# Optimization experiments

Measured on AMD Instinct MI355X. Metric: run time of the kernel, lower is better.

## Reference

```python
import jax, jax.numpy as jnp
import numpy as np
import math

D_MODEL = 2048
D_STATE = 16
EXPAND = 2
D_INNER = D_MODEL * EXPAND          # 4096
DT_RANK = math.ceil(D_MODEL / 16)   # 128
BATCH, SEQ_LEN = 2, 512


def setup_inputs() -> dict:
    key = jax.random.key(0)
    ks = jax.random.split(key, 6)
    x = jax.random.normal(ks[0], (BATCH, SEQ_LEN, D_INNER), dtype=jnp.float32)
    # A_log such that A = -exp(A_log) is a stable negative-real decay
    A_log = jnp.log(jax.random.uniform(ks[1], (D_INNER, D_STATE), minval=0.5, maxval=16.0, dtype=jnp.float32))
    D = jnp.ones((D_INNER,), dtype=jnp.float32)
    x_proj_w = 0.02 * jax.random.normal(ks[2], (DT_RANK + 2 * D_STATE, D_INNER), dtype=jnp.float32)
    dt_init_std = DT_RANK ** -0.5
    dt_proj_w = jax.random.uniform(ks[3], (D_INNER, DT_RANK), minval=-dt_init_std, maxval=dt_init_std, dtype=jnp.float32)
    # inverse-softplus init of dt bias, dt ~ loguniform[1e-3, 0.1]
    dt = jnp.exp(jax.random.uniform(ks[4], (D_INNER,), dtype=jnp.float32) * (math.log(0.1) - math.log(0.001)) + math.log(0.001))
    dt = jnp.clip(dt, 1e-4, None)
    dt_proj_b = dt + jnp.log(-jnp.expm1(-dt))
    return {"x": x, "A_log": A_log, "D": D, "x_proj_w": x_proj_w,
            "dt_proj_w": dt_proj_w, "dt_proj_b": dt_proj_b}


def reference(x, A_log, D, x_proj_w, dt_proj_w, dt_proj_b):
    # x: (b, l, d)
    A = -jnp.exp(A_log)                                  # (d, n)
    xp = jnp.einsum('bld,rd->blr', x, x_proj_w)          # (b, l, dt_rank + 2n)
    dt_in = xp[..., :DT_RANK]
    B = xp[..., DT_RANK:DT_RANK + D_STATE]               # (b, l, n)
    C = xp[..., DT_RANK + D_STATE:]                      # (b, l, n)
    dt = jax.nn.softplus(jnp.einsum('blr,dr->bld', dt_in, dt_proj_w) + dt_proj_b)  # (b, l, d)
    dA = jnp.exp(dt[..., None] * A)                      # (b, l, d, n)
    dBx = dt[..., None] * B[:, :, None, :] * x[..., None]  # (b, l, d, n)

    def step(h, inp):
        dA_t, dBx_t, C_t = inp                           # (b,d,n), (b,d,n), (b,n)
        h = dA_t * h + dBx_t
        y = jnp.einsum('bdn,bn->bd', h, C_t)
        return h, y

    h0 = jnp.zeros((x.shape[0], D_INNER, D_STATE), dtype=x.dtype)
    _, ys = jax.lax.scan(step, h0,
                         (jnp.moveaxis(dA, 1, 0), jnp.moveaxis(dBx, 1, 0), jnp.moveaxis(C, 1, 0)))
    y = jnp.moveaxis(ys, 0, 1) + D * x                   # (b, l, d)
    return y
```

## Files before the change

### kernel.cpp

```cpp
#include <hip/hip_runtime.h>
#include <math.h>

#define BATCH   2
#define SEQLEN  512
#define DI      4096
#define DS      16
#define RDT     128
#define RTOT    160
#define BL      1024

#define KSPLIT  32
#define KSL     (DI / KSPLIT)

typedef __bf16 bf16;
typedef bf16  bf16x8 __attribute__((ext_vector_type(8)));
typedef bf16  bf16x4 __attribute__((ext_vector_type(4)));
typedef float f32x4  __attribute__((ext_vector_type(4)));

__global__ __launch_bounds__(256) void cast_both(const float* __restrict__ W,
                                                 const float* __restrict__ dtw,
                                                 bf16* __restrict__ Wb,
                                                 bf16* __restrict__ dtwb) {
  const int i = blockIdx.x * 256 + threadIdx.x;
  const float4* src;
  bf16* dst;
  int j;
  if (i < RTOT * DI / 4) { src = (const float4*)W;   dst = Wb;   j = i; }
  else                   { src = (const float4*)dtw; dst = dtwb; j = i - RTOT * DI / 4; }
  float4 v = src[j];
  bf16x4 o;
  o[0] = (bf16)v.x; o[1] = (bf16)v.y; o[2] = (bf16)v.z; o[3] = (bf16)v.w;
  *(bf16x4*)(dst + 4 * (size_t)j) = o;
}

__global__ __launch_bounds__(256) void gemm_xp_mfma(const float* __restrict__ x,
                                                    const bf16* __restrict__ Wb,
                                                    float* __restrict__ part) {
  const int tid = threadIdx.x;
  const int w = tid >> 6;
  const int lane = tid & 63;
  const int m = lane & 15;
  const int q = lane >> 4;
  const int row0 = blockIdx.x * 64 + 16 * w;
  const int k0 = blockIdx.y * KSL;

  f32x4 acc[10] = {};

  const float* ap = x + (size_t)(row0 + m) * DI + k0 + 8 * q;
  const bf16*  bp = Wb + (size_t)m * DI + k0 + 8 * q;

#pragma unroll
  for (int kk = 0; kk < KSL; kk += 32) {
    float4 a0 = *(const float4*)(ap + kk);
    float4 a1 = *(const float4*)(ap + kk + 4);
    bf16x8 af;
    af[0] = (bf16)a0.x; af[1] = (bf16)a0.y; af[2] = (bf16)a0.z; af[3] = (bf16)a0.w;
    af[4] = (bf16)a1.x; af[5] = (bf16)a1.y; af[6] = (bf16)a1.z; af[7] = (bf16)a1.w;
#pragma unroll
    for (int nt = 0; nt < 10; ++nt) {
      bf16x8 bfv = *(const bf16x8*)(bp + (size_t)nt * 16 * DI + kk);
      acc[nt] = __builtin_amdgcn_mfma_f32_16x16x32_bf16(af, bfv, acc[nt], 0, 0, 0);
    }
  }

  float* p = part + (size_t)blockIdx.y * (BL * RTOT);
#pragma unroll
  for (int nt = 0; nt < 10; ++nt)
#pragma unroll
    for (int r = 0; r < 4; ++r)
      p[(size_t)(row0 + 4 * q + r) * RTOT + nt * 16 + m] = acc[nt][r];
}

__global__ __launch_bounds__(256) void reduce_xp(const float* __restrict__ part,
                                                 float* __restrict__ BCf,
                                                 bf16* __restrict__ dtinb) {
  const int o = (blockIdx.x * 256 + threadIdx.x) * 4;
  float4 s = make_float4(0.f, 0.f, 0.f, 0.f);
#pragma unroll
  for (int k = 0; k < KSPLIT; ++k) {
    float4 v = *(const float4*)&part[(size_t)k * (BL * RTOT) + o];
    s.x += v.x; s.y += v.y; s.z += v.z; s.w += v.w;
  }
  const int row = o / RTOT;
  const int col = o - row * RTOT;
  if (col < RDT) {
    bf16x4 ob;
    ob[0] = (bf16)s.x; ob[1] = (bf16)s.y; ob[2] = (bf16)s.z; ob[3] = (bf16)s.w;
    *(bf16x4*)(dtinb + (size_t)row * RDT + col) = ob;
  } else {
    *(float4*)&BCf[(size_t)row * 32 + (col - RDT)] = s;
  }
}

__device__ __forceinline__ float row16_reduce_add(float p) {
  p += __int_as_float(__builtin_amdgcn_update_dpp(
      0, __float_as_int(p), 0x111, 0xf, 0xf, true));
  p += __int_as_float(__builtin_amdgcn_update_dpp(
      0, __float_as_int(p), 0x112, 0xf, 0xf, true));
  p += __int_as_float(__builtin_amdgcn_update_dpp(
      0, __float_as_int(p), 0x114, 0xf, 0xf, true));
  p += __int_as_float(__builtin_amdgcn_update_dpp(
      0, __float_as_int(p), 0x118, 0xf, 0xf, true));
  return p;
}

#define TC  64
#define TCP 68
#define NCH (SEQLEN / TC)

__global__ __launch_bounds__(256) void scan_fused(const float* __restrict__ x,
                                                  const float* __restrict__ A_log,
                                                  const float* __restrict__ Dvec,
                                                  const float* __restrict__ BCf,
                                                  const bf16* __restrict__ dtin,
                                                  const bf16* __restrict__ dtwb,
                                                  const float* __restrict__ dtb,
                                                  float* __restrict__ out) {
  __shared__ __align__(16) float dtS[16][TCP];
  __shared__ __align__(16) float xS[16][TCP];
  __shared__ __align__(16) float BS[16][TCP];
  __shared__ __align__(16) float CS[16][TCP];
  __shared__ __align__(16) float yS[TC][16];

  const int bid = blockIdx.x;
  const int b = bid >> 8;
  const int d0 = (bid & 255) * 16;
  const int tid = threadIdx.x;
  const int n = tid & 15;
  const int dc = tid >> 4;
  const int d = d0 + dc;
  const int w = tid >> 6;
  const int m = tid & 15;
  const int q = (tid >> 4) & 3;

  const float A = -expf(A_log[d * DS + n]);
  const float Dd = Dvec[d];
  const float bias = dtb[d0 + m];

  bf16x8 bfragW[4];
#pragma unroll
  for (int k = 0; k < 4; ++k)
    bfragW[k] = *(const bf16x8*)(dtwb + (size_t)(d0 + m) * RDT + 32 * k + 8 * q);

  const int lt = tid >> 2;
  const int lf = (tid & 3) * 4;
  const int rowbase = b * SEQLEN;

  bf16x8 afrag[4];
  float4 rx, rB, rC;
  {
    const int arow = rowbase + 16 * w + m;
#pragma unroll
    for (int k = 0; k < 4; ++k)
      afrag[k] = *(const bf16x8*)(dtin + (size_t)arow * RDT + 32 * k + 8 * q);
    const int row = rowbase + lt;
    rx = *(const float4*)&x[(size_t)row * DI + d0 + lf];
    rB = *(const float4*)&BCf[row * 32 + lf];
    rC = *(const float4*)&BCf[row * 32 + 16 + lf];
  }

  float h = 0.f;

  for (int c = 0; c < NCH; ++c) {
    if (c > 0) __syncthreads();

    {
      f32x4 acc = {};
#pragma unroll
      for (int k = 0; k < 4; ++k)
        acc = __builtin_amdgcn_mfma_f32_16x16x32_bf16(afrag[k], bfragW[k], acc, 0, 0, 0);
#pragma unroll
      for (int r = 0; r < 4; ++r) {
        const float z = acc[r] + bias;
        dtS[m][16 * w + 4 * q + r] = (z > 20.f) ? z : __logf(1.f + __expf(z));
      }
    }
    {
      const float rxa[4] = {rx.x, rx.y, rx.z, rx.w};
      const float rBa[4] = {rB.x, rB.y, rB.z, rB.w};
      const float rCa[4] = {rC.x, rC.y, rC.z, rC.w};
#pragma unroll
      for (int j = 0; j < 4; ++j) {
        xS[lf + j][lt] = rxa[j];
        BS[lf + j][lt] = rBa[j];
        CS[lf + j][lt] = rCa[j];
      }
    }
    if (c > 0) {
      const int prow = rowbase + (c - 1) * TC + lt;
      float4 yv = *(const float4*)&yS[lt][lf];
      *(float4*)&out[(size_t)prow * DI + d0 + lf] = yv;
    }

    __syncthreads();

    if (c < NCH - 1) {
      const int arow = rowbase + (c + 1) * TC + 16 * w + m;
#pragma unroll
      for (int k = 0; k < 4; ++k)
        afrag[k] = *(const bf16x8*)(dtin + (size_t)arow * RDT + 32 * k + 8 * q);
      const int row = rowbase + (c + 1) * TC + lt;
      rx = *(const float4*)&x[(size_t)row * DI + d0 + lf];
      rB = *(const float4*)&BCf[row * 32 + lf];
      rC = *(const float4*)&BCf[row * 32 + 16 + lf];
    }

    for (int g = 0; g < 8; ++g) {
      const int t0 = 8 * g;
      const float4 dv0 = *(const float4*)&dtS[dc][t0];
      const float4 dv1 = *(const float4*)&dtS[dc][t0 + 4];
      const float4 xv0 = *(const float4*)&xS[dc][t0];
      const float4 xv1 = *(const float4*)&xS[dc][t0 + 4];
      const float4 Bv0 = *(const float4*)&BS[n][t0];
      const float4 Bv1 = *(const float4*)&BS[n][t0 + 4];
      const float4 Cv0 = *(const float4*)&CS[n][t0];
      const float4 Cv1 = *(const float4*)&CS[n][t0 + 4];
      const float dt[8] = {dv0.x, dv0.y, dv0.z, dv0.w, dv1.x, dv1.y, dv1.z, dv1.w};
      const float xv[8] = {xv0.x, xv0.y, xv0.z, xv0.w, xv1.x, xv1.y, xv1.z, xv1.w};
      const float Bv[8] = {Bv0.x, Bv0.y, Bv0.z, Bv0.w, Bv1.x, Bv1.y, Bv1.z, Bv1.w};
      const float Cv[8] = {Cv0.x, Cv0.y, Cv0.z, Cv0.w, Cv1.x, Cv1.y, Cv1.z, Cv1.w};

      float e[8], u[8], p[8];
#pragma unroll
      for (int j = 0; j < 8; ++j) {
        e[j] = __expf(dt[j] * A);
        u[j] = dt[j] * xv[j] * Bv[j];
      }
#pragma unroll
      for (int j = 0; j < 8; ++j) {
        h = fmaf(e[j], h, u[j]);
        p[j] = h * Cv[j];
      }
#pragma unroll
      for (int j = 0; j < 8; ++j)
        p[j] = row16_reduce_add(p[j]);
      if (n == 15) {
#pragma unroll
        for (int j = 0; j < 8; ++j)
          yS[t0 + j][dc] = fmaf(Dd, xv[j], p[j]);
      }
    }
  }

  __syncthreads();
  {
    const int prow = rowbase + (NCH - 1) * TC + lt;
    float4 yv = *(const float4*)&yS[lt][lf];
    *(float4*)&out[(size_t)prow * DI + d0 + lf] = yv;
  }
}

extern "C" void kernel_launch(void* const* d_in, const int* in_sizes, int n_in,
                              void* d_out, int out_size, void* d_ws, size_t ws_size,
                              hipStream_t stream) {
  const float* x     = (const float*)d_in[0];
  const float* A_log = (const float*)d_in[1];
  const float* Dv    = (const float*)d_in[2];
  const float* W     = (const float*)d_in[3];
  const float* dtw   = (const float*)d_in[4];
  const float* dtb   = (const float*)d_in[5];
  float* out = (float*)d_out;

  char* ws = (char*)d_ws;
  float* part  = (float*)ws;
  bf16*  Wb    = (bf16*)(ws + 20971520);
  bf16*  dtwb  = (bf16*)(ws + 22282240);
  float* BCf   = (float*)(ws + 23330816);
  bf16*  dtinb = (bf16*)(ws + 23461888);

  cast_both<<<dim3(1152), 256, 0, stream>>>(W, dtw, Wb, dtwb);
  gemm_xp_mfma<<<dim3(16, KSPLIT), 256, 0, stream>>>(x, Wb, part);
  reduce_xp<<<dim3(160), 256, 0, stream>>>(part, BCf, dtinb);
  scan_fused<<<dim3(512), 256, 0, stream>>>(x, A_log, Dv, BCf, dtinb, dtwb, dtb, out);
}
```

Baseline: 136.0 us.

## Fuse GEMM, reduce and scan into one cooperative kernel with grid syncs

Replaces the four separate launches (weight cast, split-K GEMM, reduce, scan) with a single cooperative kernel of 256 blocks of 512 threads. Each block runs two 256-thread virtual blocks, and grid.sync separates the GEMM, reduce and scan phases. The separate bf16 cast kernel is removed, so fp32 weights are converted to bf16 inline inside the GEMM and the scan. The aim is to cut launch overhead and inter-kernel gaps. In exchange it adds grid-barrier cost, twice the fp32 weight reads, and occupancy limits from the 512-thread blocks, and it falls back to three kernels if the cooperative launch fails.

```diff
diff --git a/kernel.cpp b/kernel.cpp
--- a/kernel.cpp
+++ b/kernel.cpp
@@ -1,5 +1,8 @@
 #include <hip/hip_runtime.h>
+#include <hip/hip_cooperative_groups.h>
 #include <math.h>
+
+namespace cg = cooperative_groups;
 
 #define BATCH   2
 #define SEQLEN  512
@@ -12,85 +15,14 @@
 #define KSPLIT  32
 #define KSL     (DI / KSPLIT)
 
+#define TC  64
+#define TCP 68
+#define NCH (SEQLEN / TC)
+
 typedef __bf16 bf16;
 typedef bf16  bf16x8 __attribute__((ext_vector_type(8)));
 typedef bf16  bf16x4 __attribute__((ext_vector_type(4)));
 typedef float f32x4  __attribute__((ext_vector_type(4)));
-
-__global__ __launch_bounds__(256) void cast_both(const float* __restrict__ W,
-                                                 const float* __restrict__ dtw,
-                                                 bf16* __restrict__ Wb,
-                                                 bf16* __restrict__ dtwb) {
-  const int i = blockIdx.x * 256 + threadIdx.x;
-  const float4* src;
-  bf16* dst;
-  int j;
-  if (i < RTOT * DI / 4) { src = (const float4*)W;   dst = Wb;   j = i; }
-  else                   { src = (const float4*)dtw; dst = dtwb; j = i - RTOT * DI / 4; }
-  float4 v = src[j];
-  bf16x4 o;
-  o[0] = (bf16)v.x; o[1] = (bf16)v.y; o[2] = (bf16)v.z; o[3] = (bf16)v.w;
-  *(bf16x4*)(dst + 4 * (size_t)j) = o;
-}
-
-__global__ __launch_bounds__(256) void gemm_xp_mfma(const float* __restrict__ x,
-                                                    const bf16* __restrict__ Wb,
-                                                    float* __restrict__ part) {
-  const int tid = threadIdx.x;
-  const int w = tid >> 6;
-  const int lane = tid & 63;
-  const int m = lane & 15;
-  const int q = lane >> 4;
-  const int row0 = blockIdx.x * 64 + 16 * w;
-  const int k0 = blockIdx.y * KSL;
-
-  f32x4 acc[10] = {};
-
-  const float* ap = x + (size_t)(row0 + m) * DI + k0 + 8 * q;
-  const bf16*  bp = Wb + (size_t)m * DI + k0 + 8 * q;
-
-#pragma unroll
-  for (int kk = 0; kk < KSL; kk += 32) {
-    float4 a0 = *(const float4*)(ap + kk);
-    float4 a1 = *(const float4*)(ap + kk + 4);
-    bf16x8 af;
-    af[0] = (bf16)a0.x; af[1] = (bf16)a0.y; af[2] = (bf16)a0.z; af[3] = (bf16)a0.w;
-    af[4] = (bf16)a1.x; af[5] = (bf16)a1.y; af[6] = (bf16)a1.z; af[7] = (bf16)a1.w;
-#pragma unroll
-    for (int nt = 0; nt < 10; ++nt) {
-      bf16x8 bfv = *(const bf16x8*)(bp + (size_t)nt * 16 * DI + kk);
-      acc[nt] = __builtin_amdgcn_mfma_f32_16x16x32_bf16(af, bfv, acc[nt], 0, 0, 0);
-    }
-  }
-
-  float* p = part + (size_t)blockIdx.y * (BL * RTOT);
-#pragma unroll
-  for (int nt = 0; nt < 10; ++nt)
-#pragma unroll
-    for (int r = 0; r < 4; ++r)
-      p[(size_t)(row0 + 4 * q + r) * RTOT + nt * 16 + m] = acc[nt][r];
-}
-
-__global__ __launch_bounds__(256) void reduce_xp(const float* __restrict__ part,
-                                                 float* __restrict__ BCf,
-                                                 bf16* __restrict__ dtinb) {
-  const int o = (blockIdx.x * 256 + threadIdx.x) * 4;
-  float4 s = make_float4(0.f, 0.f, 0.f, 0.f);
-#pragma unroll
-  for (int k = 0; k < KSPLIT; ++k) {
-    float4 v = *(const float4*)&part[(size_t)k * (BL * RTOT) + o];
-    s.x += v.x; s.y += v.y; s.z += v.z; s.w += v.w;
-  }
-  const int row = o / RTOT;
-  const int col = o - row * RTOT;
-  if (col < RDT) {
-    bf16x4 ob;
-    ob[0] = (bf16)s.x; ob[1] = (bf16)s.y; ob[2] = (bf16)s.z; ob[3] = (bf16)s.w;
-    *(bf16x4*)(dtinb + (size_t)row * RDT + col) = ob;
-  } else {
-    *(float4*)&BCf[(size_t)row * 32 + (col - RDT)] = s;
-  }
-}
 
 __device__ __forceinline__ float row16_reduce_add(float p) {
   p += __int_as_float(__builtin_amdgcn_update_dpp(
@@ -104,34 +36,100 @@
   return p;
 }
 
-#define TC  64
-#define TCP 68
-#define NCH (SEQLEN / TC)
-
-__global__ __launch_bounds__(256) void scan_fused(const float* __restrict__ x,
-                                                  const float* __restrict__ A_log,
-                                                  const float* __restrict__ Dvec,
-                                                  const float* __restrict__ BCf,
-                                                  const bf16* __restrict__ dtin,
-                                                  const bf16* __restrict__ dtwb,
-                                                  const float* __restrict__ dtb,
-                                                  float* __restrict__ out) {
-  __shared__ __align__(16) float dtS[16][TCP];
-  __shared__ __align__(16) float xS[16][TCP];
-  __shared__ __align__(16) float BS[16][TCP];
-  __shared__ __align__(16) float CS[16][TCP];
-  __shared__ __align__(16) float yS[TC][16];
-
-  const int bid = blockIdx.x;
-  const int b = bid >> 8;
-  const int d0 = (bid & 255) * 16;
-  const int tid = threadIdx.x;
-  const int n = tid & 15;
-  const int dc = tid >> 4;
+__device__ __forceinline__ bf16x8 cvt_bf16x8(float4 a0, float4 a1) {
+  bf16x8 r;
+  r[0] = (bf16)a0.x; r[1] = (bf16)a0.y; r[2] = (bf16)a0.z; r[3] = (bf16)a0.w;
+  r[4] = (bf16)a1.x; r[5] = (bf16)a1.y; r[6] = (bf16)a1.z; r[7] = (bf16)a1.w;
+  return r;
+}
+
+struct __align__(16) ScanLds {
+  float dtS[16][TCP];
+  float xS[16][TCP];
+  float BS[16][TCP];
+  float CS[16][TCP];
+  float yS[TC][16];
+};
+
+__device__ __forceinline__ void phaseB_gemm(const float* __restrict__ x,
+                                            const float* __restrict__ W,
+                                            float* __restrict__ part,
+                                            int vb, int t) {
+  const int w4 = t >> 6;
+  const int lane = t & 63;
+  const int m = lane & 15;
+  const int q = lane >> 4;
+  const int mb = vb >> 5;
+  const int ks = vb & 31;
+  const int row0 = mb * 64 + 16 * w4;
+  const int k0 = ks * KSL;
+
+  f32x4 acc[10] = {};
+  const float* ap = x + (size_t)(row0 + m) * DI + k0 + 8 * q;
+  const float* bp = W + (size_t)m * DI + k0 + 8 * q;
+
+#pragma unroll
+  for (int kk = 0; kk < KSL; kk += 32) {
+    float4 a0 = *(const float4*)(ap + kk);
+    float4 a1 = *(const float4*)(ap + kk + 4);
+    bf16x8 af = cvt_bf16x8(a0, a1);
+#pragma unroll
+    for (int nt = 0; nt < 10; ++nt) {
+      float4 b0 = *(const float4*)(bp + (size_t)nt * 16 * DI + kk);
+      float4 b1 = *(const float4*)(bp + (size_t)nt * 16 * DI + kk + 4);
+      bf16x8 bfv = cvt_bf16x8(b0, b1);
+      acc[nt] = __builtin_amdgcn_mfma_f32_16x16x32_bf16(af, bfv, acc[nt], 0, 0, 0);
+    }
+  }
+  float* pp = part + (size_t)ks * (BL * RTOT);
+#pragma unroll
+  for (int nt = 0; nt < 10; ++nt)
+#pragma unroll
+    for (int r = 0; r < 4; ++r)
+      pp[(size_t)(row0 + 4 * q + r) * RTOT + nt * 16 + m] = acc[nt][r];
+}
+
+__device__ __forceinline__ void phaseC_reduce(const float* __restrict__ part,
+                                              float* __restrict__ BCf,
+                                              bf16* __restrict__ dtinb,
+                                              int gtid) {
+  if (gtid >= BL * RTOT / 4) return;
+  const int o = gtid * 4;
+  float4 s = make_float4(0.f, 0.f, 0.f, 0.f);
+#pragma unroll
+  for (int k = 0; k < KSPLIT; ++k) {
+    float4 v = *(const float4*)&part[(size_t)k * (BL * RTOT) + o];
+    s.x += v.x; s.y += v.y; s.z += v.z; s.w += v.w;
+  }
+  const int row = o / RTOT;
+  const int col = o - row * RTOT;
+  if (col < RDT) {
+    bf16x4 ob;
+    ob[0] = (bf16)s.x; ob[1] = (bf16)s.y; ob[2] = (bf16)s.z; ob[3] = (bf16)s.w;
+    *(bf16x4*)(dtinb + (size_t)row * RDT + col) = ob;
+  } else {
+    *(float4*)&BCf[(size_t)row * 32 + (col - RDT)] = s;
+  }
+}
+
+__device__ __forceinline__ void phaseD_scan(ScanLds& L,
+                                            const float* __restrict__ x,
+                                            const float* __restrict__ A_log,
+                                            const float* __restrict__ Dvec,
+                                            const float* __restrict__ BCf,
+                                            const bf16* __restrict__ dtin,
+                                            const float* __restrict__ dtw,
+                                            const float* __restrict__ dtb,
+                                            float* __restrict__ out,
+                                            int group, int t) {
+  const int b = group >> 8;
+  const int d0 = (group & 255) * 16;
+  const int n = t & 15;
+  const int dc = t >> 4;
   const int d = d0 + dc;
-  const int w = tid >> 6;
-  const int m = tid & 15;
-  const int q = (tid >> 4) & 3;
+  const int w = t >> 6;
+  const int m = t & 15;
+  const int q = (t >> 4) & 3;
 
   const float A = -expf(A_log[d * DS + n]);
   const float Dd = Dvec[d];
@@ -139,11 +137,13 @@
 
   bf16x8 bfragW[4];
 #pragma unroll
-  for (int k = 0; k < 4; ++k)
-    bfragW[k] = *(const bf16x8*)(dtwb + (size_t)(d0 + m) * RDT + 32 * k + 8 * q);
-
-  const int lt = tid >> 2;
-  const int lf = (tid & 3) * 4;
+  for (int k = 0; k < 4; ++k) {
+    const float* wp = dtw + (size_t)(d0 + m) * RDT + 32 * k + 8 * q;
+    bfragW[k] = cvt_bf16x8(*(const float4*)wp, *(const float4*)(wp + 4));
+  }
+
+  const int lt = t >> 2;
+  const int lf = (t & 3) * 4;
   const int rowbase = b * SEQLEN;
 
   bf16x8 afrag[4];
@@ -172,7 +172,7 @@
 #pragma unroll
       for (int r = 0; r < 4; ++r) {
         const float z = acc[r] + bias;
-        dtS[m][16 * w + 4 * q + r] = (z > 20.f) ? z : __logf(1.f + __expf(z));
+        L.dtS[m][16 * w + 4 * q + r] = (z > 20.f) ? z : __logf(1.f + __expf(z));
       }
     }
     {
@@ -181,14 +181,14 @@
       const float rCa[4] = {rC.x, rC.y, rC.z, rC.w};
 #pragma unroll
       for (int j = 0; j < 4; ++j) {
-        xS[lf + j][lt] = rxa[j];
-        BS[lf + j][lt] = rBa[j];
-        CS[lf + j][lt] = rCa[j];
+        L.xS[lf + j][lt] = rxa[j];
+        L.BS[lf + j][lt] = rBa[j];
+        L.CS[lf + j][lt] = rCa[j];
       }
     }
     if (c > 0) {
       const int prow = rowbase + (c - 1) * TC + lt;
-      float4 yv = *(const float4*)&yS[lt][lf];
+      float4 yv = *(const float4*)&L.yS[lt][lf];
       *(float4*)&out[(size_t)prow * DI + d0 + lf] = yv;
     }
 
@@ -207,14 +207,14 @@
 
     for (int g = 0; g < 8; ++g) {
       const int t0 = 8 * g;
-      const float4 dv0 = *(const float4*)&dtS[dc][t0];
-      const float4 dv1 = *(const float4*)&dtS[dc][t0 + 4];
-      const float4 xv0 = *(const float4*)&xS[dc][t0];
-      const float4 xv1 = *(const float4*)&xS[dc][t0 + 4];
-      const float4 Bv0 = *(const float4*)&BS[n][t0];
-      const float4 Bv1 = *(const float4*)&BS[n][t0 + 4];
-      const float4 Cv0 = *(const float4*)&CS[n][t0];
-      const float4 Cv1 = *(const float4*)&CS[n][t0 + 4];
+      const float4 dv0 = *(const float4*)&L.dtS[dc][t0];
+      const float4 dv1 = *(const float4*)&L.dtS[dc][t0 + 4];
+      const float4 xv0 = *(const float4*)&L.xS[dc][t0];
+      const float4 xv1 = *(const float4*)&L.xS[dc][t0 + 4];
+      const float4 Bv0 = *(const float4*)&L.BS[n][t0];
+      const float4 Bv1 = *(const float4*)&L.BS[n][t0 + 4];
+      const float4 Cv0 = *(const float4*)&L.CS[n][t0];
+      const float4 Cv1 = *(const float4*)&L.CS[n][t0 + 4];
       const float dt[8] = {dv0.x, dv0.y, dv0.z, dv0.w, dv1.x, dv1.y, dv1.z, dv1.w};
       const float xv[8] = {xv0.x, xv0.y, xv0.z, xv0.w, xv1.x, xv1.y, xv1.z, xv1.w};
       const float Bv[8] = {Bv0.x, Bv0.y, Bv0.z, Bv0.w, Bv1.x, Bv1.y, Bv1.z, Bv1.w};
@@ -237,7 +237,7 @@
       if (n == 15) {
 #pragma unroll
         for (int j = 0; j < 8; ++j)
-          yS[t0 + j][dc] = fmaf(Dd, xv[j], p[j]);
+          L.yS[t0 + j][dc] = fmaf(Dd, xv[j], p[j]);
       }
     }
   }
@@ -245,9 +245,60 @@
   __syncthreads();
   {
     const int prow = rowbase + (NCH - 1) * TC + lt;
-    float4 yv = *(const float4*)&yS[lt][lf];
+    float4 yv = *(const float4*)&L.yS[lt][lf];
     *(float4*)&out[(size_t)prow * DI + d0 + lf] = yv;
   }
+}
+
+__global__ __launch_bounds__(512, 2) void fused_all(
+    const float* __restrict__ x,     const float* __restrict__ A_log,
+    const float* __restrict__ Dvec,  const float* __restrict__ W,
+    const float* __restrict__ dtw,   const float* __restrict__ dtb,
+    float* __restrict__ part,        float* __restrict__ BCf,
+    bf16* __restrict__ dtinb,        float* __restrict__ out) {
+  __shared__ ScanLds L[2];
+  const int tid = threadIdx.x;
+  const int bid = blockIdx.x;
+  const int half = tid >> 8;
+  const int t = tid & 255;
+
+  cg::grid_group grid = cg::this_grid();
+
+  phaseB_gemm(x, W, part, bid * 2 + half, t);
+
+  __threadfence();
+  grid.sync();
+
+  phaseC_reduce(part, BCf, dtinb, bid * 512 + tid);
+
+  __threadfence();
+  grid.sync();
+
+  phaseD_scan(L[half], x, A_log, Dvec, BCf, dtinb, dtw, dtb, out,
+              bid * 2 + half, t);
+}
+
+__global__ __launch_bounds__(512, 2) void fb_gemm(const float* __restrict__ x,
+                                                  const float* __restrict__ W,
+                                                  float* __restrict__ part) {
+  phaseB_gemm(x, W, part, blockIdx.x * 2 + (threadIdx.x >> 8), threadIdx.x & 255);
+}
+
+__global__ __launch_bounds__(512) void fb_reduce(const float* __restrict__ part,
+                                                 float* __restrict__ BCf,
+                                                 bf16* __restrict__ dtinb) {
+  phaseC_reduce(part, BCf, dtinb, blockIdx.x * 512 + threadIdx.x);
+}
+
+__global__ __launch_bounds__(512, 2) void fb_scan(
+    const float* __restrict__ x, const float* __restrict__ A_log,
+    const float* __restrict__ Dvec, const float* __restrict__ BCf,
+    const bf16* __restrict__ dtin, const float* __restrict__ dtw,
+    const float* __restrict__ dtb, float* __restrict__ out) {
+  __shared__ ScanLds L[2];
+  const int half = threadIdx.x >> 8;
+  phaseD_scan(L[half], x, A_log, Dvec, BCf, dtin, dtw, dtb, out,
+              blockIdx.x * 2 + half, threadIdx.x & 255);
 }
 
 extern "C" void kernel_launch(void* const* d_in, const int* in_sizes, int n_in,
@@ -263,13 +314,17 @@
 
   char* ws = (char*)d_ws;
   float* part  = (float*)ws;
-  bf16*  Wb    = (bf16*)(ws + 20971520);
-  bf16*  dtwb  = (bf16*)(ws + 22282240);
-  float* BCf   = (float*)(ws + 23330816);
-  bf16*  dtinb = (bf16*)(ws + 23461888);
-
-  cast_both<<<dim3(1152), 256, 0, stream>>>(W, dtw, Wb, dtwb);
-  gemm_xp_mfma<<<dim3(16, KSPLIT), 256, 0, stream>>>(x, Wb, part);
-  reduce_xp<<<dim3(160), 256, 0, stream>>>(part, BCf, dtinb);
-  scan_fused<<<dim3(512), 256, 0, stream>>>(x, A_log, Dv, BCf, dtinb, dtwb, dtb, out);
-}
+  float* BCf   = (float*)(ws + 20971520);
+  bf16*  dtinb = (bf16*)(ws + 21102592);
+
+  void* args[] = {(void*)&x, (void*)&A_log, (void*)&Dv, (void*)&W, (void*)&dtw,
+                  (void*)&dtb, (void*)&part, (void*)&BCf, (void*)&dtinb, (void*)&out};
+  hipError_t err = hipLaunchCooperativeKernel((void*)fused_all, dim3(256),
+                                              dim3(512), args, 0, stream);
+  if (err != hipSuccess) {
+    (void)hipGetLastError();
+    fb_gemm<<<dim3(256), 512, 0, stream>>>(x, W, part);
+    fb_reduce<<<dim3(80), 512, 0, stream>>>(part, BCf, dtinb);
+    fb_scan<<<dim3(256), 512, 0, stream>>>(x, A_log, Dv, BCf, dtinb, dtw, dtb, out);
+  }
+}
```

New measurement: 343.6 us. 2.53x slower.

## Fuse weight cast, split-K GEMM and reduction into one in-block reduced GEMM

Applied to the files above, without the earlier changes.

Drops the separate weight-cast and partial-sum reduction kernels. The x-projection GEMM now runs as 64 blocks of 512 threads, where each of the 8 waves covers a 512-wide K slice and the partial sums are combined through shared memory in a tree before writing BCf and dt_in directly. The fp32 weights are converted to bf16 on the fly in both the GEMM and the scan kernel. This removes two launches and about 20MB of partial-sum traffic. In exchange, the GEMM grid shrinks from 512 blocks to 64, so many CUs may sit idle, and W is re-read in fp32 by every block.

```diff
diff --git a/kernel.cpp b/kernel.cpp
--- a/kernel.cpp
+++ b/kernel.cpp
@@ -9,111 +9,125 @@
 #define RTOT    160
 #define BL      1024
 
-#define KSPLIT  32
-#define KSL     (DI / KSPLIT)
+#define TC  64
+#define TCP 68
+#define NCH (SEQLEN / TC)
 
 typedef __bf16 bf16;
 typedef bf16  bf16x8 __attribute__((ext_vector_type(8)));
 typedef bf16  bf16x4 __attribute__((ext_vector_type(4)));
 typedef float f32x4  __attribute__((ext_vector_type(4)));
 
-__global__ __launch_bounds__(256) void cast_both(const float* __restrict__ W,
-                                                 const float* __restrict__ dtw,
-                                                 bf16* __restrict__ Wb,
-                                                 bf16* __restrict__ dtwb) {
-  const int i = blockIdx.x * 256 + threadIdx.x;
-  const float4* src;
-  bf16* dst;
-  int j;
-  if (i < RTOT * DI / 4) { src = (const float4*)W;   dst = Wb;   j = i; }
-  else                   { src = (const float4*)dtw; dst = dtwb; j = i - RTOT * DI / 4; }
-  float4 v = src[j];
-  bf16x4 o;
-  o[0] = (bf16)v.x; o[1] = (bf16)v.y; o[2] = (bf16)v.z; o[3] = (bf16)v.w;
-  *(bf16x4*)(dst + 4 * (size_t)j) = o;
-}
-
-__global__ __launch_bounds__(256) void gemm_xp_mfma(const float* __restrict__ x,
-                                                    const bf16* __restrict__ Wb,
-                                                    float* __restrict__ part) {
+__device__ __forceinline__ float row16_reduce_add(float p) {
+  p += __int_as_float(__builtin_amdgcn_update_dpp(
+      0, __float_as_int(p), 0x111, 0xf, 0xf, true));
+  p += __int_as_float(__builtin_amdgcn_update_dpp(
+      0, __float_as_int(p), 0x112, 0xf, 0xf, true));
+  p += __int_as_float(__builtin_amdgcn_update_dpp(
+      0, __float_as_int(p), 0x114, 0xf, 0xf, true));
+  p += __int_as_float(__builtin_amdgcn_update_dpp(
+      0, __float_as_int(p), 0x118, 0xf, 0xf, true));
+  return p;
+}
+
+__device__ __forceinline__ bf16x8 cvt_bf16x8(float4 a0, float4 a1) {
+  bf16x8 r;
+  r[0] = (bf16)a0.x; r[1] = (bf16)a0.y; r[2] = (bf16)a0.z; r[3] = (bf16)a0.w;
+  r[4] = (bf16)a1.x; r[5] = (bf16)a1.y; r[6] = (bf16)a1.z; r[7] = (bf16)a1.w;
+  return r;
+}
+
+__global__ __launch_bounds__(512) void gemm_fused(const float* __restrict__ x,
+                                                  const float* __restrict__ W,
+                                                  float* __restrict__ BCf,
+                                                  bf16* __restrict__ dtinb) {
+  __shared__ __align__(16) float img[4][16][164];
   const int tid = threadIdx.x;
   const int w = tid >> 6;
   const int lane = tid & 63;
   const int m = lane & 15;
   const int q = lane >> 4;
-  const int row0 = blockIdx.x * 64 + 16 * w;
-  const int k0 = blockIdx.y * KSL;
+  const int row0 = blockIdx.x * 16;
+  const int k0 = w * 512;
 
   f32x4 acc[10] = {};
-
   const float* ap = x + (size_t)(row0 + m) * DI + k0 + 8 * q;
-  const bf16*  bp = Wb + (size_t)m * DI + k0 + 8 * q;
-
-#pragma unroll
-  for (int kk = 0; kk < KSL; kk += 32) {
+  const float* bp = W + (size_t)m * DI + k0 + 8 * q;
+
+#pragma unroll 4
+  for (int kk = 0; kk < 512; kk += 32) {
     float4 a0 = *(const float4*)(ap + kk);
     float4 a1 = *(const float4*)(ap + kk + 4);
-    bf16x8 af;
-    af[0] = (bf16)a0.x; af[1] = (bf16)a0.y; af[2] = (bf16)a0.z; af[3] = (bf16)a0.w;
-    af[4] = (bf16)a1.x; af[5] = (bf16)a1.y; af[6] = (bf16)a1.z; af[7] = (bf16)a1.w;
+    bf16x8 af = cvt_bf16x8(a0, a1);
 #pragma unroll
     for (int nt = 0; nt < 10; ++nt) {
-      bf16x8 bfv = *(const bf16x8*)(bp + (size_t)nt * 16 * DI + kk);
+      float4 b0 = *(const float4*)(bp + (size_t)nt * 16 * DI + kk);
+      float4 b1 = *(const float4*)(bp + (size_t)nt * 16 * DI + kk + 4);
+      bf16x8 bfv = cvt_bf16x8(b0, b1);
       acc[nt] = __builtin_amdgcn_mfma_f32_16x16x32_bf16(af, bfv, acc[nt], 0, 0, 0);
     }
   }
 
-  float* p = part + (size_t)blockIdx.y * (BL * RTOT);
-#pragma unroll
-  for (int nt = 0; nt < 10; ++nt)
-#pragma unroll
-    for (int r = 0; r < 4; ++r)
-      p[(size_t)(row0 + 4 * q + r) * RTOT + nt * 16 + m] = acc[nt][r];
-}
-
-__global__ __launch_bounds__(256) void reduce_xp(const float* __restrict__ part,
-                                                 float* __restrict__ BCf,
-                                                 bf16* __restrict__ dtinb) {
-  const int o = (blockIdx.x * 256 + threadIdx.x) * 4;
-  float4 s = make_float4(0.f, 0.f, 0.f, 0.f);
-#pragma unroll
-  for (int k = 0; k < KSPLIT; ++k) {
-    float4 v = *(const float4*)&part[(size_t)k * (BL * RTOT) + o];
-    s.x += v.x; s.y += v.y; s.z += v.z; s.w += v.w;
-  }
-  const int row = o / RTOT;
-  const int col = o - row * RTOT;
-  if (col < RDT) {
-    bf16x4 ob;
-    ob[0] = (bf16)s.x; ob[1] = (bf16)s.y; ob[2] = (bf16)s.z; ob[3] = (bf16)s.w;
-    *(bf16x4*)(dtinb + (size_t)row * RDT + col) = ob;
-  } else {
-    *(float4*)&BCf[(size_t)row * 32 + (col - RDT)] = s;
-  }
-}
-
-__device__ __forceinline__ float row16_reduce_add(float p) {
-  p += __int_as_float(__builtin_amdgcn_update_dpp(
-      0, __float_as_int(p), 0x111, 0xf, 0xf, true));
-  p += __int_as_float(__builtin_amdgcn_update_dpp(
-      0, __float_as_int(p), 0x112, 0xf, 0xf, true));
-  p += __int_as_float(__builtin_amdgcn_update_dpp(
-      0, __float_as_int(p), 0x114, 0xf, 0xf, true));
-  p += __int_as_float(__builtin_amdgcn_update_dpp(
-      0, __float_as_int(p), 0x118, 0xf, 0xf, true));
-  return p;
-}
-
-#define TC  64
-#define TCP 68
-#define NCH (SEQLEN / TC)
+  if (w >= 4) {
+#pragma unroll
+    for (int nt = 0; nt < 10; ++nt)
+#pragma unroll
+      for (int r = 0; r < 4; ++r)
+        img[w - 4][4 * q + r][nt * 16 + m] = acc[nt][r];
+  }
+  __syncthreads();
+  if (w < 4) {
+#pragma unroll
+    for (int nt = 0; nt < 10; ++nt)
+#pragma unroll
+      for (int r = 0; r < 4; ++r)
+        acc[nt][r] += img[w][4 * q + r][nt * 16 + m];
+  }
+  __syncthreads();
+  if (w == 2 || w == 3) {
+#pragma unroll
+    for (int nt = 0; nt < 10; ++nt)
+#pragma unroll
+      for (int r = 0; r < 4; ++r)
+        img[w - 2][4 * q + r][nt * 16 + m] = acc[nt][r];
+  }
+  __syncthreads();
+  if (w < 2) {
+#pragma unroll
+    for (int nt = 0; nt < 10; ++nt)
+#pragma unroll
+      for (int r = 0; r < 4; ++r)
+        acc[nt][r] += img[w][4 * q + r][nt * 16 + m];
+  }
+  __syncthreads();
+  if (w == 1) {
+#pragma unroll
+    for (int nt = 0; nt < 10; ++nt)
+#pragma unroll
+      for (int r = 0; r < 4; ++r)
+        img[0][4 * q + r][nt * 16 + m] = acc[nt][r];
+  }
+  __syncthreads();
+  if (w == 0) {
+#pragma unroll
+    for (int nt = 0; nt < 10; ++nt)
+#pragma unroll
+      for (int r = 0; r < 4; ++r) {
+        const float v = acc[nt][r] + img[0][4 * q + r][nt * 16 + m];
+        const int row = row0 + 4 * q + r;
+        const int col = nt * 16 + m;
+        if (col < RDT) dtinb[(size_t)row * RDT + col] = (bf16)v;
+        else           BCf[(size_t)row * 32 + (col - RDT)] = v;
+      }
+  }
+}
 
 __global__ __launch_bounds__(256) void scan_fused(const float* __restrict__ x,
                                                   const float* __restrict__ A_log,
                                                   const float* __restrict__ Dvec,
                                                   const float* __restrict__ BCf,
                                                   const bf16* __restrict__ dtin,
-                                                  const bf16* __restrict__ dtwb,
+                                                  const float* __restrict__ dtw,
                                                   const float* __restrict__ dtb,
                                                   float* __restrict__ out) {
   __shared__ __align__(16) float dtS[16][TCP];
@@ -139,8 +153,10 @@
 
   bf16x8 bfragW[4];
 #pragma unroll
-  for (int k = 0; k < 4; ++k)
-    bfragW[k] = *(const bf16x8*)(dtwb + (size_t)(d0 + m) * RDT + 32 * k + 8 * q);
+  for (int k = 0; k < 4; ++k) {
+    const float* wp = dtw + (size_t)(d0 + m) * RDT + 32 * k + 8 * q;
+    bfragW[k] = cvt_bf16x8(*(const float4*)wp, *(const float4*)(wp + 4));
+  }
 
   const int lt = tid >> 2;
   const int lf = (tid & 3) * 4;
@@ -262,14 +278,9 @@
   float* out = (float*)d_out;
 
   char* ws = (char*)d_ws;
-  float* part  = (float*)ws;
-  bf16*  Wb    = (bf16*)(ws + 20971520);
-  bf16*  dtwb  = (bf16*)(ws + 22282240);
-  float* BCf   = (float*)(ws + 23330816);
-  bf16*  dtinb = (bf16*)(ws + 23461888);
-
-  cast_both<<<dim3(1152), 256, 0, stream>>>(W, dtw, Wb, dtwb);
-  gemm_xp_mfma<<<dim3(16, KSPLIT), 256, 0, stream>>>(x, Wb, part);
-  reduce_xp<<<dim3(160), 256, 0, stream>>>(part, BCf, dtinb);
-  scan_fused<<<dim3(512), 256, 0, stream>>>(x, A_log, Dv, BCf, dtinb, dtwb, dtb, out);
-}
+  float* BCf   = (float*)ws;
+  bf16*  dtinb = (bf16*)(ws + 131072);
+
+  gemm_fused<<<dim3(64), 512, 0, stream>>>(x, W, BCf, dtinb);
+  scan_fused<<<dim3(512), 256, 0, stream>>>(x, A_log, Dv, BCf, dtinb, dtw, dtb, out);
+}
```

Result: slower. 194.2 us (+42.9%).

## Fuse weight bf16 casts into GEMM and scan, double scan chunk length

Applied to the files above, without the earlier changes.

Drops the separate cast kernel: the x_proj GEMM now loads fp32 weights and converts them to bf16 in registers, with all B loads batched before the MFMAs behind a scheduling barrier. The scan kernel likewise converts dt_proj weights in place. The scan chunk grows from 64 to 128 timesteps, halving the number of chunk iterations and their barriers, with the staging loads reorganised. This removes one launch and a weight round-trip through memory, at the cost of more LDS and registers per block and redundant per-block conversion work.

```diff
diff --git a/kernel.cpp b/kernel.cpp
--- a/kernel.cpp
+++ b/kernel.cpp
@@ -10,31 +10,37 @@
 #define BL      1024
 
 #define KSPLIT  32
-#define KSL     (DI / KSPLIT)
+
+#define TC  128
+#define TCP 132
+#define NCH (SEQLEN / TC)
 
 typedef __bf16 bf16;
 typedef bf16  bf16x8 __attribute__((ext_vector_type(8)));
 typedef bf16  bf16x4 __attribute__((ext_vector_type(4)));
 typedef float f32x4  __attribute__((ext_vector_type(4)));
 
-__global__ __launch_bounds__(256) void cast_both(const float* __restrict__ W,
-                                                 const float* __restrict__ dtw,
-                                                 bf16* __restrict__ Wb,
-                                                 bf16* __restrict__ dtwb) {
-  const int i = blockIdx.x * 256 + threadIdx.x;
-  const float4* src;
-  bf16* dst;
-  int j;
-  if (i < RTOT * DI / 4) { src = (const float4*)W;   dst = Wb;   j = i; }
-  else                   { src = (const float4*)dtw; dst = dtwb; j = i - RTOT * DI / 4; }
-  float4 v = src[j];
-  bf16x4 o;
-  o[0] = (bf16)v.x; o[1] = (bf16)v.y; o[2] = (bf16)v.z; o[3] = (bf16)v.w;
-  *(bf16x4*)(dst + 4 * (size_t)j) = o;
-}
-
-__global__ __launch_bounds__(256) void gemm_xp_mfma(const float* __restrict__ x,
-                                                    const bf16* __restrict__ Wb,
+__device__ __forceinline__ float row16_reduce_add(float p) {
+  p += __int_as_float(__builtin_amdgcn_update_dpp(
+      0, __float_as_int(p), 0x111, 0xf, 0xf, true));
+  p += __int_as_float(__builtin_amdgcn_update_dpp(
+      0, __float_as_int(p), 0x112, 0xf, 0xf, true));
+  p += __int_as_float(__builtin_amdgcn_update_dpp(
+      0, __float_as_int(p), 0x114, 0xf, 0xf, true));
+  p += __int_as_float(__builtin_amdgcn_update_dpp(
+      0, __float_as_int(p), 0x118, 0xf, 0xf, true));
+  return p;
+}
+
+__device__ __forceinline__ bf16x8 cvt_bf16x8(float4 a0, float4 a1) {
+  bf16x8 r;
+  r[0] = (bf16)a0.x; r[1] = (bf16)a0.y; r[2] = (bf16)a0.z; r[3] = (bf16)a0.w;
+  r[4] = (bf16)a1.x; r[5] = (bf16)a1.y; r[6] = (bf16)a1.z; r[7] = (bf16)a1.w;
+  return r;
+}
+
+__global__ __launch_bounds__(256, 2) void gemm_part(const float* __restrict__ x,
+                                                    const float* __restrict__ W,
                                                     float* __restrict__ part) {
   const int tid = threadIdx.x;
   const int w = tid >> 6;
@@ -42,33 +48,39 @@
   const int m = lane & 15;
   const int q = lane >> 4;
   const int row0 = blockIdx.x * 64 + 16 * w;
-  const int k0 = blockIdx.y * KSL;
+  const int k0 = blockIdx.y * 128;
 
   f32x4 acc[10] = {};
-
   const float* ap = x + (size_t)(row0 + m) * DI + k0 + 8 * q;
-  const bf16*  bp = Wb + (size_t)m * DI + k0 + 8 * q;
-
-#pragma unroll
-  for (int kk = 0; kk < KSL; kk += 32) {
+  const float* bp = W + (size_t)m * DI + k0 + 8 * q;
+
+#pragma unroll
+  for (int ks = 0; ks < 4; ++ks) {
+    const int kk = 32 * ks;
     float4 a0 = *(const float4*)(ap + kk);
     float4 a1 = *(const float4*)(ap + kk + 4);
-    bf16x8 af;
-    af[0] = (bf16)a0.x; af[1] = (bf16)a0.y; af[2] = (bf16)a0.z; af[3] = (bf16)a0.w;
-    af[4] = (bf16)a1.x; af[5] = (bf16)a1.y; af[6] = (bf16)a1.z; af[7] = (bf16)a1.w;
+    float4 b0[10], b1[10];
 #pragma unroll
     for (int nt = 0; nt < 10; ++nt) {
-      bf16x8 bfv = *(const bf16x8*)(bp + (size_t)nt * 16 * DI + kk);
+      const float* bpn = bp + (size_t)nt * 16 * DI + kk;
+      b0[nt] = *(const float4*)(bpn);
+      b1[nt] = *(const float4*)(bpn + 4);
+    }
+    __builtin_amdgcn_sched_barrier(0);
+    bf16x8 af = cvt_bf16x8(a0, a1);
+#pragma unroll
+    for (int nt = 0; nt < 10; ++nt) {
+      bf16x8 bfv = cvt_bf16x8(b0[nt], b1[nt]);
       acc[nt] = __builtin_amdgcn_mfma_f32_16x16x32_bf16(af, bfv, acc[nt], 0, 0, 0);
     }
   }
 
-  float* p = part + (size_t)blockIdx.y * (BL * RTOT);
+  float* pp = part + (size_t)blockIdx.y * (BL * RTOT);
 #pragma unroll
   for (int nt = 0; nt < 10; ++nt)
 #pragma unroll
     for (int r = 0; r < 4; ++r)
-      p[(size_t)(row0 + 4 * q + r) * RTOT + nt * 16 + m] = acc[nt][r];
+      pp[(size_t)(row0 + 4 * q + r) * RTOT + nt * 16 + m] = acc[nt][r];
 }
 
 __global__ __launch_bounds__(256) void reduce_xp(const float* __restrict__ part,
@@ -92,30 +104,14 @@
   }
 }
 
-__device__ __forceinline__ float row16_reduce_add(float p) {
-  p += __int_as_float(__builtin_amdgcn_update_dpp(
-      0, __float_as_int(p), 0x111, 0xf, 0xf, true));
-  p += __int_as_float(__builtin_amdgcn_update_dpp(
-      0, __float_as_int(p), 0x112, 0xf, 0xf, true));
-  p += __int_as_float(__builtin_amdgcn_update_dpp(
-      0, __float_as_int(p), 0x114, 0xf, 0xf, true));
-  p += __int_as_float(__builtin_amdgcn_update_dpp(
-      0, __float_as_int(p), 0x118, 0xf, 0xf, true));
-  return p;
-}
-
-#define TC  64
-#define TCP 68
-#define NCH (SEQLEN / TC)
-
-__global__ __launch_bounds__(256) void scan_fused(const float* __restrict__ x,
-                                                  const float* __restrict__ A_log,
-                                                  const float* __restrict__ Dvec,
-                                                  const float* __restrict__ BCf,
-                                                  const bf16* __restrict__ dtin,
-                                                  const bf16* __restrict__ dtwb,
-                                                  const float* __restrict__ dtb,
-                                                  float* __restrict__ out) {
+__global__ __launch_bounds__(256, 2) void scan_fused(const float* __restrict__ x,
+                                                     const float* __restrict__ A_log,
+                                                     const float* __restrict__ Dvec,
+                                                     const float* __restrict__ BCf,
+                                                     const bf16* __restrict__ dtin,
+                                                     const float* __restrict__ dtw,
+                                                     const float* __restrict__ dtb,
+                                                     float* __restrict__ out) {
   __shared__ __align__(16) float dtS[16][TCP];
   __shared__ __align__(16) float xS[16][TCP];
   __shared__ __align__(16) float BS[16][TCP];
@@ -139,24 +135,31 @@
 
   bf16x8 bfragW[4];
 #pragma unroll
-  for (int k = 0; k < 4; ++k)
-    bfragW[k] = *(const bf16x8*)(dtwb + (size_t)(d0 + m) * RDT + 32 * k + 8 * q);
-
-  const int lt = tid >> 2;
-  const int lf = (tid & 3) * 4;
+  for (int k = 0; k < 4; ++k) {
+    const float* wp = dtw + (size_t)(d0 + m) * RDT + 32 * k + 8 * q;
+    bfragW[k] = cvt_bf16x8(*(const float4*)wp, *(const float4*)(wp + 4));
+  }
+
+  const int lt = tid >> 1;
+  const int half = tid & 1;
   const int rowbase = b * SEQLEN;
 
-  bf16x8 afrag[4];
-  float4 rx, rB, rC;
+  bf16x8 afrag[2][4];
+  float4 rx[2], rbc[4];
   {
-    const int arow = rowbase + 16 * w + m;
-#pragma unroll
-    for (int k = 0; k < 4; ++k)
-      afrag[k] = *(const bf16x8*)(dtin + (size_t)arow * RDT + 32 * k + 8 * q);
+#pragma unroll
+    for (int tt = 0; tt < 2; ++tt) {
+      const int arow = rowbase + 32 * w + 16 * tt + m;
+#pragma unroll
+      for (int k = 0; k < 4; ++k)
+        afrag[tt][k] = *(const bf16x8*)(dtin + (size_t)arow * RDT + 32 * k + 8 * q);
+    }
     const int row = rowbase + lt;
-    rx = *(const float4*)&x[(size_t)row * DI + d0 + lf];
-    rB = *(const float4*)&BCf[row * 32 + lf];
-    rC = *(const float4*)&BCf[row * 32 + 16 + lf];
+    rx[0] = *(const float4*)&x[(size_t)row * DI + d0 + 8 * half];
+    rx[1] = *(const float4*)&x[(size_t)row * DI + d0 + 8 * half + 4];
+#pragma unroll
+    for (int j = 0; j < 4; ++j)
+      rbc[j] = *(const float4*)&BCf[row * 32 + 16 * half + 4 * j];
   }
 
   float h = 0.f;
@@ -164,48 +167,63 @@
   for (int c = 0; c < NCH; ++c) {
     if (c > 0) __syncthreads();
 
-    {
+#pragma unroll
+    for (int tt = 0; tt < 2; ++tt) {
       f32x4 acc = {};
 #pragma unroll
       for (int k = 0; k < 4; ++k)
-        acc = __builtin_amdgcn_mfma_f32_16x16x32_bf16(afrag[k], bfragW[k], acc, 0, 0, 0);
+        acc = __builtin_amdgcn_mfma_f32_16x16x32_bf16(afrag[tt][k], bfragW[k], acc, 0, 0, 0);
 #pragma unroll
       for (int r = 0; r < 4; ++r) {
         const float z = acc[r] + bias;
-        dtS[m][16 * w + 4 * q + r] = (z > 20.f) ? z : __logf(1.f + __expf(z));
+        dtS[m][32 * w + 16 * tt + 4 * q + r] = (z > 20.f) ? z : __logf(1.f + __expf(z));
       }
     }
     {
-      const float rxa[4] = {rx.x, rx.y, rx.z, rx.w};
-      const float rBa[4] = {rB.x, rB.y, rB.z, rB.w};
-      const float rCa[4] = {rC.x, rC.y, rC.z, rC.w};
-#pragma unroll
-      for (int j = 0; j < 4; ++j) {
-        xS[lf + j][lt] = rxa[j];
-        BS[lf + j][lt] = rBa[j];
-        CS[lf + j][lt] = rCa[j];
-      }
+      const float rxa[8] = {rx[0].x, rx[0].y, rx[0].z, rx[0].w,
+                            rx[1].x, rx[1].y, rx[1].z, rx[1].w};
+#pragma unroll
+      for (int j = 0; j < 8; ++j)
+        xS[8 * half + j][lt] = rxa[j];
+    }
+    {
+      float* basep = half ? &CS[0][0] : &BS[0][0];
+      const float rb[16] = {rbc[0].x, rbc[0].y, rbc[0].z, rbc[0].w,
+                            rbc[1].x, rbc[1].y, rbc[1].z, rbc[1].w,
+                            rbc[2].x, rbc[2].y, rbc[2].z, rbc[2].w,
+                            rbc[3].x, rbc[3].y, rbc[3].z, rbc[3].w};
+#pragma unroll
+      for (int j = 0; j < 16; ++j)
+        basep[j * TCP + lt] = rb[j];
     }
     if (c > 0) {
       const int prow = rowbase + (c - 1) * TC + lt;
-      float4 yv = *(const float4*)&yS[lt][lf];
-      *(float4*)&out[(size_t)prow * DI + d0 + lf] = yv;
+      float4 y0 = *(const float4*)&yS[lt][8 * half];
+      float4 y1 = *(const float4*)&yS[lt][8 * half + 4];
+      *(float4*)&out[(size_t)prow * DI + d0 + 8 * half] = y0;
+      *(float4*)&out[(size_t)prow * DI + d0 + 8 * half + 4] = y1;
     }
 
     __syncthreads();
 
     if (c < NCH - 1) {
-      const int arow = rowbase + (c + 1) * TC + 16 * w + m;
-#pragma unroll
-      for (int k = 0; k < 4; ++k)
-        afrag[k] = *(const bf16x8*)(dtin + (size_t)arow * RDT + 32 * k + 8 * q);
-      const int row = rowbase + (c + 1) * TC + lt;
-      rx = *(const float4*)&x[(size_t)row * DI + d0 + lf];
-      rB = *(const float4*)&BCf[row * 32 + lf];
-      rC = *(const float4*)&BCf[row * 32 + 16 + lf];
-    }
-
-    for (int g = 0; g < 8; ++g) {
+      const int cb = (c + 1) * TC;
+#pragma unroll
+      for (int tt = 0; tt < 2; ++tt) {
+        const int arow = rowbase + cb + 32 * w + 16 * tt + m;
+#pragma unroll
+        for (int k = 0; k < 4; ++k)
+          afrag[tt][k] = *(const bf16x8*)(dtin + (size_t)arow * RDT + 32 * k + 8 * q);
+      }
+      const int row = rowbase + cb + lt;
+      rx[0] = *(const float4*)&x[(size_t)row * DI + d0 + 8 * half];
+      rx[1] = *(const float4*)&x[(size_t)row * DI + d0 + 8 * half + 4];
+#pragma unroll
+      for (int j = 0; j < 4; ++j)
+        rbc[j] = *(const float4*)&BCf[row * 32 + 16 * half + 4 * j];
+    }
+
+    for (int g = 0; g < 16; ++g) {
       const int t0 = 8 * g;
       const float4 dv0 = *(const float4*)&dtS[dc][t0];
       const float4 dv1 = *(const float4*)&dtS[dc][t0 + 4];
@@ -245,8 +263,10 @@
   __syncthreads();
   {
     const int prow = rowbase + (NCH - 1) * TC + lt;
-    float4 yv = *(const float4*)&yS[lt][lf];
-    *(float4*)&out[(size_t)prow * DI + d0 + lf] = yv;
+    float4 y0 = *(const float4*)&yS[lt][8 * half];
+    float4 y1 = *(const float4*)&yS[lt][8 * half + 4];
+    *(float4*)&out[(size_t)prow * DI + d0 + 8 * half] = y0;
+    *(float4*)&out[(size_t)prow * DI + d0 + 8 * half + 4] = y1;
   }
 }
 
@@ -263,13 +283,10 @@
 
   char* ws = (char*)d_ws;
   float* part  = (float*)ws;
-  bf16*  Wb    = (bf16*)(ws + 20971520);
-  bf16*  dtwb  = (bf16*)(ws + 22282240);
-  float* BCf   = (float*)(ws + 23330816);
-  bf16*  dtinb = (bf16*)(ws + 23461888);
-
-  cast_both<<<dim3(1152), 256, 0, stream>>>(W, dtw, Wb, dtwb);
-  gemm_xp_mfma<<<dim3(16, KSPLIT), 256, 0, stream>>>(x, Wb, part);
+  float* BCf   = (float*)(ws + 20971520);
+  bf16*  dtinb = (bf16*)(ws + 21102592);
+
+  gemm_part<<<dim3(16, KSPLIT), 256, 0, stream>>>(x, W, part);
   reduce_xp<<<dim3(160), 256, 0, stream>>>(part, BCf, dtinb);
-  scan_fused<<<dim3(512), 256, 0, stream>>>(x, A_log, Dv, BCf, dtinb, dtwb, dtb, out);
-}
+  scan_fused<<<dim3(512), 256, 0, stream>>>(x, A_log, Dv, BCf, dtinb, dtw, dtb, out);
+}
```

Result: slower. 147.0 us (+8.1%).
